# Performance work log

Measured on AMD Instinct MI355X. Metric: run time of the kernel, lower is better.

Reference implementation:

```python
import jax, jax.numpy as jnp
import numpy as np

LATENT, TARGET, EMB_SCALE = 2048, 64, 0.1
STEPS_IGNORE, STEPS_PREDICT = 2, 3


def conv(x, w, b, stride=(1, 1), padding=((0, 0), (0, 0))):
    y = jax.lax.conv_general_dilated(x, w, stride, padding,
                                     dimension_numbers=('NCHW', 'OIHW', 'NCHW'))
    return y + b[None, :, None, None]


def setup_inputs() -> dict:
    key = jax.random.key(0)
    ks = jax.random.split(key, 24)
    B = 64
    inp = {}
    inp['images'] = jax.random.normal(ks[0], (B, 3, 256, 256), jnp.float32)
    inp['rnd'] = jax.random.randint(ks[1], (B * 49,), 0, 16, jnp.int32)
    s = lambda *sh: 1.0 / np.sqrt(np.prod(sh[1:]))
    # stand-in encoder: conv3->256 k8 s8, relu, conv256->2048 1x1, relu, global mean pool
    inp['enc_w1'] = jax.random.normal(ks[2], (256, 3, 8, 8), jnp.float32) * s(256, 3, 8, 8)
    inp['enc_b1'] = jnp.zeros((256,), jnp.float32)
    inp['enc_w2'] = jax.random.normal(ks[3], (LATENT, 256, 1, 1), jnp.float32) * s(LATENT, 256)
    inp['enc_b2'] = jnp.zeros((LATENT,), jnp.float32)
    # PixelCNN: 5 residual blocks, each 4 convs
    inp['pc_w1'] = jax.random.normal(ks[4], (5, 256, LATENT, 1, 1), jnp.float32) * s(0, LATENT)
    inp['pc_b1'] = jnp.zeros((5, 256), jnp.float32)
    inp['pc_w2'] = jax.random.normal(ks[5], (5, 256, 256, 1, 3), jnp.float32) * s(0, 256 * 3)
    inp['pc_b2'] = jnp.zeros((5, 256), jnp.float32)
    inp['pc_w3'] = jax.random.normal(ks[6], (5, 256, 256, 2, 1), jnp.float32) * s(0, 256 * 2)
    inp['pc_b3'] = jnp.zeros((5, 256), jnp.float32)
    inp['pc_w4'] = jax.random.normal(ks[7], (5, LATENT, 256, 1, 1), jnp.float32) * s(0, 256)
    inp['pc_b4'] = jnp.zeros((5, LATENT), jnp.float32)
    inp['z2t_w'] = jax.random.normal(ks[8], (TARGET, LATENT, 1, 1), jnp.float32) * s(0, LATENT)
    inp['z2t_b'] = jnp.zeros((TARGET,), jnp.float32)
    inp['c2p_w'] = jax.random.normal(ks[9], (STEPS_PREDICT, TARGET, LATENT, 1, 1), jnp.float32) * s(0, LATENT)
    inp['c2p_b'] = jnp.zeros((STEPS_PREDICT, TARGET), jnp.float32)
    return inp


def _forward(images, enc_w1, enc_b1, enc_w2, enc_b2,
             pc_w1, pc_b1, pc_w2, pc_b2, pc_w3, pc_b3, pc_w4, pc_b4,
             z2t_w, z2t_b, c2p_w, c2p_b, rnd):
    B = images.shape[0]
    # ---- patch extraction: (B,3,256,256) -> (B*49,3,64,64), r-major then c ----
    patches = jnp.stack([images[:, :, r * 32:r * 32 + 64, c * 32:c * 32 + 64]
                         for r in range(7) for c in range(7)], axis=1)
    patches = patches.reshape(-1, 3, 64, 64)
    N = patches.shape[0]
    # ---- vectorized random border masking (replaces per-patch python loop) ----
    r = (rnd // 4).astype(jnp.int32)           # (N,)
    c = (rnd % 4).astype(jnp.int32)
    idx = jnp.arange(64, dtype=jnp.int32)
    row_ok = (idx[None, :] >= r[:, None]) & (idx[None, :] < r[:, None] + 60)  # (N,64)
    col_ok = (idx[None, :] >= c[:, None]) & (idx[None, :] < c[:, None] + 60)
    mask = row_ok[:, None, :, None] & col_ok[:, None, None, :]                # (N,1,64,64)
    patches = jnp.where(mask, patches, jnp.float32(-1.0))
    # ---- stand-in encoder (resnet_v1 replaced by small conv stack) ----
    h = jax.nn.relu(conv(patches, enc_w1, enc_b1, stride=(8, 8)))  # (N,256,8,8)
    h = jax.nn.relu(conv(h, enc_w2, enc_b2))                        # (N,2048,8,8)
    latents = h.mean(axis=(2, 3))                                   # (N,2048)
    latents = latents.reshape(B, 7, 7, LATENT).transpose(0, 3, 1, 2)  # (B,2048,7,7)
    # ---- PixelCNN context ----
    x = latents
    for k in range(5):
        y = jax.nn.relu(conv(x, pc_w1[k], pc_b1[k]))
        y = jax.nn.relu(conv(y, pc_w2[k], pc_b2[k], padding=((0, 0), (1, 1))))
        y = jax.nn.relu(conv(y, pc_w3[k], pc_b3[k], padding=((1, 0), (0, 0))))
        y = conv(y, pc_w4[k], pc_b4[k])
        x = jax.nn.relu(y + x)
    context = x
    # ---- contrastive loss ----
    targets = conv(latents, z2t_w, z2t_b).transpose(0, 2, 3, 1).reshape(-1, TARGET)  # (B*49,64)
    col_dim, row_dim = 7, 7
    loss = jnp.float32(0.0)
    for i in range(STEPS_IGNORE, STEPS_IGNORE + STEPS_PREDICT):
        col_dim_i = col_dim - i - 1
        total = B * col_dim_i * row_dim
        preds = conv(context, c2p_w[i - STEPS_IGNORE], c2p_b[i - STEPS_IGNORE])
        preds = preds[:, :, :-(i + 1), :] * EMB_SCALE
        preds = preds.transpose(0, 2, 3, 1).reshape(-1, TARGET)  # (total,64)
        logits = preds @ targets.T                                # (total, B*49)
        ar = jnp.arange(total)
        b_idx = ar // (col_dim_i * row_dim)
        col = ar % (col_dim_i * row_dim)
        labels = b_idx * (col_dim * row_dim) + (i + 1) * row_dim + col
        lsm = jax.nn.log_softmax(logits, axis=-1)
        loss = loss + (-lsm[ar, labels]).mean()
    return loss, latents.mean(axis=(2, 3))


def reference(images, rnd, enc_w1, enc_b1, enc_w2, enc_b2,
              pc_w1, pc_b1, pc_w2, pc_b2, pc_w3, pc_b3, pc_w4, pc_b4,
              z2t_w, z2t_b, c2p_w, c2p_b):
    return _forward(images, enc_w1, enc_b1, enc_w2, enc_b2,
                    pc_w1, pc_b1, pc_w2, pc_b2, pc_w3, pc_b3, pc_w4, pc_b4,
                    z2t_w, z2t_b, c2p_w, c2p_b, rnd)
```

## Files before the change

kernel.cpp:

```cpp
#include <hip/hip_runtime.h>
#include <hip/hip_bf16.h>
#include <cstdint>
#include <cstddef>

typedef __attribute__((ext_vector_type(8))) short short8;
typedef __attribute__((ext_vector_type(4))) short short4v;
typedef __attribute__((ext_vector_type(4))) float f32x4;

__device__ __forceinline__ float bf2f(unsigned short u) {
  union { unsigned int i; float f; } v; v.i = ((unsigned int)u) << 16; return v.f;
}
__device__ __forceinline__ unsigned short f2bf(float f) {
  union { float f; unsigned int i; } v; v.f = f;
  unsigned int x = v.i;
  return (unsigned short)((x + 0x7fffu + ((x >> 16) & 1u)) >> 16);
}
__device__ __forceinline__ f32x4 mfma16(short8 a, short8 b, f32x4 c) {
  return __builtin_amdgcn_mfma_f32_16x16x32_bf16(a, b, c, 0, 0, 0);
}
__device__ __forceinline__ void gload16(const void* src, void* dst) {
  __builtin_amdgcn_global_load_lds(
      (const __attribute__((address_space(1))) unsigned int*)src,
      (__attribute__((address_space(3))) unsigned int*)dst, 16, 0, 0);
}

__device__ __forceinline__ void cvt4(const float* __restrict__ src,
                                     unsigned short* __restrict__ dst, int i) {
  float4 v = reinterpret_cast<const float4*>(src)[i];
  short4v o;
  o[0] = (short)f2bf(v.x); o[1] = (short)f2bf(v.y);
  o[2] = (short)f2bf(v.z); o[3] = (short)f2bf(v.w);
  reinterpret_cast<short4v*>(dst)[i] = o;
}

__global__ __launch_bounds__(256) void k_prep(
    const float* __restrict__ enc_w1, const float* __restrict__ enc_w2,
    const float* __restrict__ pc_w1, const float* __restrict__ pc_w4,
    const float* __restrict__ z2t_w, const float* __restrict__ c2p_w,
    const float* __restrict__ pc_w2, const float* __restrict__ pc_w3,
    unsigned short* __restrict__ w1b, unsigned short* __restrict__ w2b,
    unsigned short* __restrict__ pcw1b, unsigned short* __restrict__ pcw4b,
    unsigned short* __restrict__ z2tb, unsigned short* __restrict__ c2pb,
    unsigned short* __restrict__ w2t, unsigned short* __restrict__ w3t)
{
  const int b = blockIdx.x, tid = threadIdx.x;
  if (b < 48)        cvt4(enc_w1, w1b,   b * 256 + tid);
  else if (b < 560)  cvt4(enc_w2, w2b,   (b - 48) * 256 + tid);
  else if (b < 3120) cvt4(pc_w1,  pcw1b, (b - 560) * 256 + tid);
  else if (b < 5680) cvt4(pc_w4,  pcw4b, (b - 3120) * 256 + tid);
  else if (b < 5808) cvt4(z2t_w,  z2tb,  (b - 5680) * 256 + tid);
  else if (b < 6192) cvt4(c2p_w,  c2pb,  (b - 5808) * 256 + tid);
  else if (b < 10032) {
    const int e = (b - 6192) * 256 + tid;
    const int k5 = e / 196608, r = e % 196608;
    const int co = r / 768, kk = r % 768, d = kk >> 8, ci = kk & 255;
    w2t[e] = f2bf(pc_w2[((size_t)(k5 * 256 + co) * 256 + ci) * 3 + d]);
  } else {
    const int e = (b - 10032) * 256 + tid;
    const int k5 = e / 131072, r = e % 131072;
    const int co = r >> 9, kk = r & 511, s = kk >> 8, ci = kk & 255;
    w3t[e] = f2bf(pc_w3[((size_t)(k5 * 256 + co) * 256 + ci) * 2 + s]);
  }
}

__global__ __launch_bounds__(256) void k_enc2(
    const unsigned short* __restrict__ H1, const unsigned short* __restrict__ w2b,
    const float* __restrict__ b2, unsigned short* __restrict__ xout, int gbase)
{
  __shared__ char lds[32768];
  char* At = lds;
  char* Bt = lds + 16384;
  const int tid = threadIdx.x;
  const int nwg = gridDim.x;
  int bid = blockIdx.x;
  int l = bid;
  if ((nwg & 7) == 0) { const int cpx = nwg >> 3; l = (bid & 7) * cpx + (bid >> 3); }
  const int m0 = (l & 15) * 128;
  const int by = l >> 4;
  const int w = tid >> 6, lane = tid & 63, lr = lane & 15, lg = lane >> 4;
  const int wm = w & 1, wn = w >> 1;
  const int srow = lane >> 3, sslot = lane & 7;
  f32x4 acc[4][4];
  for (int i = 0; i < 4; i++) for (int j = 0; j < 4; j++) acc[i][j] = (f32x4)0.f;
  for (int kb = 0; kb < 4; kb++) {
    __syncthreads();
#pragma unroll
    for (int c = 0; c < 4; c++) {
      const int rbase = w * 32 + c * 8;
      const int row = rbase + srow;
      gload16(w2b + (size_t)(m0 + row) * 256 + kb * 64 + ((sslot ^ (row & 7)) * 8),
              At + rbase * 128);
    }
#pragma unroll
    for (int c = 0; c < 4; c++) {
      const int rbase = w * 32 + c * 8;
      const int row = rbase + srow;
      gload16(H1 + (size_t)(by * 128 + row) * 256 + kb * 64 + ((sslot ^ (row & 7)) * 8),
              Bt + rbase * 128);
    }
    __syncthreads();
#pragma unroll
    for (int kk = 0; kk < 2; kk++) {
      const int gg = kk * 4 + lg;
      short8 bb[4];
#pragma unroll
      for (int nt = 0; nt < 4; nt++) {
        const int row = wn * 64 + nt * 16 + lr;
        bb[nt] = *reinterpret_cast<const short8*>(Bt + row * 128 + ((gg ^ (row & 7)) * 16));
      }
#pragma unroll
      for (int cot = 0; cot < 4; cot++) {
        const int row = wm * 64 + cot * 16 + lr;
        const short8 a = *reinterpret_cast<const short8*>(At + row * 128 + ((gg ^ (row & 7)) * 16));
#pragma unroll
        for (int nt = 0; nt < 4; nt++)
          acc[cot][nt] = mfma16(a, bb[nt], acc[cot][nt]);
      }
    }
  }
  const int n = gbase + by * 2 + wn;
#pragma unroll
  for (int cot = 0; cot < 4; cot++) {
    const int cob = m0 + wm * 64 + cot * 16 + lg * 4;
    float4 bi = *reinterpret_cast<const float4*>(b2 + cob);
    const float bv[4] = { bi.x, bi.y, bi.z, bi.w };
    float s[4] = { 0.f, 0.f, 0.f, 0.f };
#pragma unroll
    for (int nt = 0; nt < 4; nt++)
#pragma unroll
      for (int r = 0; r < 4; r++)
        s[r] += fmaxf(acc[cot][nt][r] + bv[r], 0.f);
#pragma unroll
    for (int r = 0; r < 4; r++)
#pragma unroll
      for (int mk = 1; mk < 16; mk <<= 1)
        s[r] += __shfl_xor(s[r], mk, 64);
    if (lr == 0) {
      short4v o;
#pragma unroll
      for (int r = 0; r < 4; r++) o[r] = (short)f2bf(s[r] * (1.f / 64.f));
      *reinterpret_cast<short4v*>(xout + (size_t)n * 2048 + cob) = o;
    }
  }
}

__global__ __launch_bounds__(256) void k_out2(const unsigned short* __restrict__ x,
                                              float* __restrict__ out) {
  const int ch = blockIdx.x * 256 + threadIdx.x;
  const int b = blockIdx.y;
  float s = 0.f;
  for (int p = 0; p < 49; p++) s += bf2f(x[(size_t)(b * 49 + p) * 2048 + ch]);
  out[1 + b * 2048 + ch] = s * (1.f / 49.f);
}

template<int M_BLK, int MODE, bool BIAS, bool RELU, bool RESID, bool SCALE, bool OBF16>
__global__ __launch_bounds__(256) void k_gemm(
    const unsigned short* __restrict__ in, const unsigned short* __restrict__ W,
    const float* __restrict__ bias, float* __restrict__ outf,
    unsigned short* __restrict__ outb, const unsigned short* __restrict__ res,
    int M, int K, int bstride, int aux, float scale,
    int wzs, int bzs, int ozs,
    const float* __restrict__ img, const int* __restrict__ rndp)
{
  constexpr int MF = M_BLK / 64;
  constexpr int AG = M_BLK * 8;
  constexpr int CHA = M_BLK / 32;
  __shared__ char ldsb[(M_BLK + 64) * 128];
  char* At = ldsb;
  char* Bt = ldsb + M_BLK * 128;
  const int tid = threadIdx.x;
  const int z = blockIdx.z;
  W += (size_t)z * wzs;
  if (BIAS) bias += (size_t)z * bzs;
  const int m0 = blockIdx.x * M_BLK;
  const int n0 = blockIdx.y * 64;
  const int w = tid >> 6, lane = tid & 63, lr = lane & 15, lg = lane >> 4;
  const int srow = lane >> 3, sslot = lane & 7;
  int pb = 0, pR = 0, pC = 0, roff = 0, coff = 0;
  if constexpr (MODE == 4) {
    const int pn = aux + blockIdx.y;
    pb = pn / 49; const int prc = pn % 49; pR = prc / 7; pC = prc % 7;
    const int rv = rndp[pn];
    roff = rv >> 2; coff = rv & 3;
  }
  f32x4 acc[MF][4];
  for (int mf = 0; mf < MF; mf++) for (int nt = 0; nt < 4; nt++) acc[mf][nt] = (f32x4)0.f;
  const int KB = K >> 6;
  for (int kb = 0; kb < KB; kb++) {
    __syncthreads();
#pragma unroll
    for (int c = 0; c < CHA; c++) {
      const int rbase = w * (M_BLK / 4) + c * 8;
      const int row = rbase + srow;
      gload16(W + (size_t)(m0 + row) * K + kb * 64 + ((sslot ^ (row & 7)) * 8),
              At + rbase * 128);
    }
    if constexpr (MODE == 0 || MODE == 3) {
#pragma unroll
      for (int c = 0; c < 2; c++) {
        const int rbase = w * 16 + c * 8;
        const int row = rbase + srow;
        int n = n0 + row;
        if constexpr (MODE == 3) n = (n / aux) * 49 + (n % aux);
        gload16(in + (size_t)n * bstride + kb * 64 + ((sslot ^ (row & 7)) * 8),
                Bt + rbase * 128);
      }
    } else {
      for (int g = AG + tid; g < AG + 512; g += 256) {
        const int h = g - AG, row = h >> 3, slot = h & 7;
        const int n = n0 + row;
        const int k = kb * 64 + slot * 8;
        short8 v = (short8)(short)0;
        if constexpr (MODE == 1) {
          const int d = k >> 8, ci = k & 255;
          const int wp = n % 7 + d - 1;
          if ((unsigned)wp <= 6u)
            v = *reinterpret_cast<const short8*>(in + (size_t)(n + d - 1) * 256 + ci);
        } else if constexpr (MODE == 2) {
          const int s2 = k >> 8, ci = k & 255;
          const int hh = (n % 49) / 7;
          if (hh + s2 >= 1)
            v = *reinterpret_cast<const short8*>(in + (size_t)(n + (s2 - 1) * 7) * 256 + ci);
        } else {
          const int p = row;
          const int gr = kb * 8 + slot;
          const int ci = gr >> 3, ky = gr & 7;
          const int oy = p >> 3, ox = p & 7;
          const int y = oy * 8 + ky;
          const float* src = img + (((size_t)(pb * 3 + ci) * 256 + (size_t)(pR * 32 + y)) * 256
                                    + pC * 32 + ox * 8);
          float4 v0 = *reinterpret_cast<const float4*>(src);
          float4 v1 = *reinterpret_cast<const float4*>(src + 4);
          const bool rok = (y >= roff) && (y < roff + 60);
          float vals[8] = { v0.x, v0.y, v0.z, v0.w, v1.x, v1.y, v1.z, v1.w };
          const int x0 = ox * 8;
#pragma unroll
          for (int q = 0; q < 8; q++) {
            const int xx = x0 + q;
            const bool ok = rok && (xx >= coff) && (xx < coff + 60);
            v[q] = (short)f2bf(ok ? vals[q] : -1.0f);
          }
        }
        *reinterpret_cast<short8*>(Bt + row * 128 + ((slot ^ (row & 7)) * 16)) = v;
      }
    }
    __syncthreads();
#pragma unroll
    for (int kk = 0; kk < 2; kk++) {
      short8 a[MF], bb[4];
      const int gg = kk * 4 + lg;
#pragma unroll
      for (int mf = 0; mf < MF; mf++) {
        const int row = w * (M_BLK / 4) + mf * 16 + lr;
        a[mf] = *reinterpret_cast<const short8*>(At + row * 128 + ((gg ^ (row & 7)) * 16));
      }
#pragma unroll
      for (int nt = 0; nt < 4; nt++) {
        const int row = nt * 16 + lr;
        bb[nt] = *reinterpret_cast<const short8*>(Bt + row * 128 + ((gg ^ (row & 7)) * 16));
      }
#pragma unroll
      for (int mf = 0; mf < MF; mf++)
#pragma unroll
        for (int nt = 0; nt < 4; nt++)
          acc[mf][nt] = mfma16(a[mf], bb[nt], acc[mf][nt]);
    }
  }
#pragma unroll
  for (int mf = 0; mf < MF; mf++) {
    const int mb = m0 + w * (M_BLK / 4) + mf * 16 + lg * 4;
    float bv[4] = {0.f, 0.f, 0.f, 0.f};
    if constexpr (BIAS) {
      float4 t4 = *reinterpret_cast<const float4*>(bias + mb);
      bv[0] = t4.x; bv[1] = t4.y; bv[2] = t4.z; bv[3] = t4.w;
    }
#pragma unroll
    for (int nt = 0; nt < 4; nt++) {
      const size_t nn = (size_t)(n0 + nt * 16 + lr);
      const size_t off = nn * (size_t)M + mb + (size_t)z * ozs;
      float v[4];
#pragma unroll
      for (int r = 0; r < 4; r++) {
        v[r] = acc[mf][nt][r] + bv[r];
        if (SCALE) v[r] *= scale;
      }
      if (RESID) {
        short4v rv = *reinterpret_cast<const short4v*>(res + off);
#pragma unroll
        for (int r = 0; r < 4; r++) v[r] += bf2f((unsigned short)rv[r]);
      }
#pragma unroll
      for (int r = 0; r < 4; r++) if (RELU) v[r] = fmaxf(v[r], 0.f);
      if (OBF16) {
        short4v o;
#pragma unroll
        for (int r = 0; r < 4; r++) o[r] = (short)f2bf(v[r]);
        *reinterpret_cast<short4v*>(outb + off) = o;
      } else {
        float4 o; o.x = v[0]; o.y = v[1]; o.z = v[2]; o.w = v[3];
        *reinterpret_cast<float4*>(outf + off) = o;
      }
    }
  }
}

__global__ __launch_bounds__(256) void k_lse(const float* __restrict__ logits,
                                             float* __restrict__ lossr,
                                             int cd7, int base, int lab7)
{
  __shared__ float redM[256], redS[256];
  const int r = blockIdx.x, tid = threadIdx.x;
  const float4* row = reinterpret_cast<const float4*>(logits + (size_t)r * 3136);
  float m = -1e30f, s = 0.f;
  for (int i = tid; i < 784; i += 256) {
    float4 v4 = row[i];
    float vv[4] = { v4.x, v4.y, v4.z, v4.w };
#pragma unroll
    for (int q = 0; q < 4; q++) {
      const float nm = fmaxf(m, vv[q]);
      s = s * __expf(m - nm) + __expf(vv[q] - nm);
      m = nm;
    }
  }
  redM[tid] = m; redS[tid] = s;
  for (int off = 128; off > 0; off >>= 1) {
    __syncthreads();
    if (tid < off) {
      const float m2 = redM[tid + off], s2 = redS[tid + off];
      const float nm = fmaxf(redM[tid], m2);
      redS[tid] = redS[tid] * __expf(redM[tid] - nm) + s2 * __expf(m2 - nm);
      redM[tid] = nm;
    }
  }
  __syncthreads();
  if (tid == 0) {
    const int b = r / cd7, hw = r % cd7;
    const int lab = b * 49 + hw + lab7;
    lossr[base + r] = (redM[0] + __logf(redS[0])) - logits[(size_t)r * 3136 + lab];
  }
}

__global__ __launch_bounds__(256) void k_loss_final(const float* __restrict__ lossr,
                                                    float* __restrict__ out) {
  __shared__ float red[256];
  const int tid = threadIdx.x;
  float s = 0.f;
  for (int i = tid; i < 4032; i += 256) {
    const float wgt = (i < 1792) ? (1.f / 1792.f) : ((i < 3136) ? (1.f / 1344.f) : (1.f / 896.f));
    s += lossr[i] * wgt;
  }
  red[tid] = s;
  for (int off = 128; off > 0; off >>= 1) {
    __syncthreads();
    if (tid < off) red[tid] += red[tid + off];
  }
  if (tid == 0) out[0] = red[0];
}

extern "C" void kernel_launch(void* const* d_in, const int* in_sizes, int n_in,
                              void* d_out, int out_size, void* d_ws, size_t ws_size,
                              hipStream_t stream)
{
  (void)in_sizes; (void)n_in; (void)out_size;
  const float* images = (const float*)d_in[0];
  const int*   rnd    = (const int*)d_in[1];
  const float* enc_w1 = (const float*)d_in[2];
  const float* enc_b1 = (const float*)d_in[3];
  const float* enc_w2 = (const float*)d_in[4];
  const float* enc_b2 = (const float*)d_in[5];
  const float* pc_w1  = (const float*)d_in[6];
  const float* pc_b1  = (const float*)d_in[7];
  const float* pc_w2  = (const float*)d_in[8];
  const float* pc_b2  = (const float*)d_in[9];
  const float* pc_w3  = (const float*)d_in[10];
  const float* pc_b3  = (const float*)d_in[11];
  const float* pc_w4  = (const float*)d_in[12];
  const float* pc_b4  = (const float*)d_in[13];
  const float* z2t_w  = (const float*)d_in[14];
  const float* z2t_b  = (const float*)d_in[15];
  const float* c2p_w  = (const float*)d_in[16];
  const float* c2p_b  = (const float*)d_in[17];
  float* out = (float*)d_out;
  char* ws = (char*)d_ws;

  unsigned short* w1b    = (unsigned short*)(ws + 0);
  unsigned short* w2b    = (unsigned short*)(ws + 98304);
  unsigned short* z2tb   = (unsigned short*)(ws + 1146880);
  unsigned short* c2pb   = (unsigned short*)(ws + 1409024);
  unsigned short* w2t    = (unsigned short*)(ws + 2195456);
  unsigned short* w3t    = (unsigned short*)(ws + 4161536);
  unsigned short* targ   = (unsigned short*)(ws + 5472256);
  unsigned short* predsb = (unsigned short*)(ws + 5873664);
  float*          lossr  = (float*)(ws + 7077888);
  unsigned short* y1b    = (unsigned short*)(ws + 7094016);
  unsigned short* y2b    = (unsigned short*)(ws + 8699648);
  unsigned short* pcw1b  = (unsigned short*)(ws + 10305280);
  unsigned short* pcw4b  = (unsigned short*)(ws + 15548160);
  unsigned short* xbuf   = (unsigned short*)(ws + 20791040);
  float*          logits = (float*)(ws + 10305280);

  k_prep<<<12592, 256, 0, stream>>>(enc_w1, enc_w2, pc_w1, pc_w4, z2t_w, c2p_w,
                                    pc_w2, pc_w3,
                                    w1b, w2b, pcw1b, pcw4b, z2tb, c2pb, w2t, w3t);

  const size_t h1_off = 33636352;
  const size_t per_patch = 64 * 256 * 2;
  unsigned short* H1;
  int CH;
  if (ws_size > h1_off + 2 * per_patch) {
    size_t avail = (ws_size - h1_off) / per_patch;
    CH = (int)(avail > 3136 ? 3136 : avail) & ~1;
    H1 = (unsigned short*)(ws + h1_off);
  } else {
    H1 = y1b;
    CH = 98;
  }
  for (int base = 0; base < 3136; base += CH) {
    const int c = (3136 - base) < CH ? (3136 - base) : CH;
    k_gemm<256, 4, true, true, false, false, true><<<dim3(1, c), 256, 0, stream>>>(
        nullptr, w1b, enc_b1, nullptr, H1, nullptr, 256, 192, 0, base, 1.f,
        0, 0, 0, images, rnd);
    k_enc2<<<16 * (c / 2), 256, 0, stream>>>(H1, w2b, enc_b2, xbuf, base);
  }

  k_out2<<<dim3(8, 64), 256, 0, stream>>>(xbuf, out);
  k_gemm<64, 0, true, false, false, false, true><<<dim3(1, 49), 256, 0, stream>>>(
      xbuf, z2tb, z2t_b, nullptr, targ, nullptr, 64, 2048, 2048, 0, 1.f, 0, 0, 0,
      nullptr, nullptr);

  for (int k = 0; k < 5; k++) {
    k_gemm<64, 0, true, true, false, false, true><<<dim3(4, 49), 256, 0, stream>>>(
        xbuf, pcw1b + (size_t)k * 524288, pc_b1 + k * 256, nullptr, y1b, nullptr,
        256, 2048, 2048, 0, 1.f, 0, 0, 0, nullptr, nullptr);
    k_gemm<64, 1, true, true, false, false, true><<<dim3(4, 49), 256, 0, stream>>>(
        y1b, w2t + (size_t)k * 196608, pc_b2 + k * 256, nullptr, y2b, nullptr,
        256, 768, 256, 0, 1.f, 0, 0, 0, nullptr, nullptr);
    k_gemm<64, 2, true, true, false, false, true><<<dim3(4, 49), 256, 0, stream>>>(
        y2b, w3t + (size_t)k * 131072, pc_b3 + k * 256, nullptr, y1b, nullptr,
        256, 512, 256, 0, 1.f, 0, 0, 0, nullptr, nullptr);
    k_gemm<128, 0, true, true, true, false, true><<<dim3(16, 49), 256, 0, stream>>>(
        y1b, pcw4b + (size_t)k * 524288, pc_b4 + k * 2048, nullptr, xbuf, xbuf,
        2048, 256, 256, 0, 1.f, 0, 0, 0, nullptr, nullptr);
  }

  k_gemm<64, 0, true, false, false, true, true><<<dim3(1, 49, 3), 256, 0, stream>>>(
      xbuf, c2pb, c2p_b, nullptr, predsb, nullptr, 64, 2048, 2048, 0, 0.1f,
      131072, 64, 200704, nullptr, nullptr);

  const int cd7a[3] = {28, 21, 14};
  const int basea[3] = {0, 1792, 3136};
  for (int ip = 0; ip < 3; ip++) {
    const int rows = cd7a[ip] * 64;
    k_gemm<64, 3, false, false, false, false, false><<<dim3(49, rows / 64), 256, 0, stream>>>(
        predsb + (size_t)ip * 200704, targ, nullptr, logits, nullptr, nullptr,
        3136, 64, 64, cd7a[ip], 1.f, 0, 0, 0, nullptr, nullptr);
    k_lse<<<rows, 256, 0, stream>>>(logits, lossr, cd7a[ip], basea[ip], 7 * (ip + 3));
  }
  k_loss_final<<<1, 256, 0, stream>>>(lossr, out);
}
```

Baseline: 723.9 us.

## Double-buffer LDS tiles in encoder and GEMM kernels to overlap loads with MFMA

Adds ping-pong LDS buffers to k_enc2 and to the k_gemm modes that load B tiles with direct global-to-LDS copies (modes 0 and 3). The next K-tile is issued into the spare buffer before the MFMA loop on the current tile, and one barrier per iteration replaces two. The aim is to hide global load latency behind the matrix math. In exchange, LDS use per block doubles, which can cut how many workgroups fit on a CU. The modes that gather B tiles in software keep the single-buffer path.

```diff
diff --git a/kernel.cpp b/kernel.cpp
--- a/kernel.cpp
+++ b/kernel.cpp
@@ -67,9 +67,7 @@
     const unsigned short* __restrict__ H1, const unsigned short* __restrict__ w2b,
     const float* __restrict__ b2, unsigned short* __restrict__ xout, int gbase)
 {
-  __shared__ char lds[32768];
-  char* At = lds;
-  char* Bt = lds + 16384;
+  __shared__ char lds[2][32768];
   const int tid = threadIdx.x;
   const int nwg = gridDim.x;
   int bid = blockIdx.x;
@@ -82,8 +80,10 @@
   const int srow = lane >> 3, sslot = lane & 7;
   f32x4 acc[4][4];
   for (int i = 0; i < 4; i++) for (int j = 0; j < 4; j++) acc[i][j] = (f32x4)0.f;
-  for (int kb = 0; kb < 4; kb++) {
-    __syncthreads();
+
+  auto STAGE = [&](int buf, int kb) {
+    char* At = lds[buf];
+    char* Bt = lds[buf] + 16384;
 #pragma unroll
     for (int c = 0; c < 4; c++) {
       const int rbase = w * 32 + c * 8;
@@ -98,7 +98,15 @@
       gload16(H1 + (size_t)(by * 128 + row) * 256 + kb * 64 + ((sslot ^ (row & 7)) * 8),
               Bt + rbase * 128);
     }
-    __syncthreads();
+  };
+
+  STAGE(0, 0);
+  __syncthreads();
+  int cur = 0;
+  for (int kb = 0; kb < 4; kb++) {
+    if (kb < 3) STAGE(cur ^ 1, kb + 1);
+    char* At = lds[cur];
+    char* Bt = lds[cur] + 16384;
 #pragma unroll
     for (int kk = 0; kk < 2; kk++) {
       const int gg = kk * 4 + lg;
@@ -117,6 +125,8 @@
           acc[cot][nt] = mfma16(a, bb[nt], acc[cot][nt]);
       }
     }
+    __syncthreads();
+    cur ^= 1;
   }
   const int n = gbase + by * 2 + wn;
 #pragma unroll
@@ -165,9 +175,9 @@
   constexpr int MF = M_BLK / 64;
   constexpr int AG = M_BLK * 8;
   constexpr int CHA = M_BLK / 32;
-  __shared__ char ldsb[(M_BLK + 64) * 128];
-  char* At = ldsb;
-  char* Bt = ldsb + M_BLK * 128;
+  constexpr bool DBUF = (MODE == 0 || MODE == 3);
+  constexpr int BUF = (M_BLK + 64) * 128;
+  __shared__ char ldsb[(DBUF ? 2 : 1) * BUF];
   const int tid = threadIdx.x;
   const int z = blockIdx.z;
   W += (size_t)z * wzs;
@@ -186,8 +196,8 @@
   f32x4 acc[MF][4];
   for (int mf = 0; mf < MF; mf++) for (int nt = 0; nt < 4; nt++) acc[mf][nt] = (f32x4)0.f;
   const int KB = K >> 6;
-  for (int kb = 0; kb < KB; kb++) {
-    __syncthreads();
+
+  auto stageA = [&](char* At, int kb) {
 #pragma unroll
     for (int c = 0; c < CHA; c++) {
       const int rbase = w * (M_BLK / 4) + c * 8;
@@ -195,7 +205,32 @@
       gload16(W + (size_t)(m0 + row) * K + kb * 64 + ((sslot ^ (row & 7)) * 8),
               At + rbase * 128);
     }
-    if constexpr (MODE == 0 || MODE == 3) {
+  };
+  auto compute = [&](const char* At, const char* Bt) {
+#pragma unroll
+    for (int kk = 0; kk < 2; kk++) {
+      short8 a[MF], bb[4];
+      const int gg = kk * 4 + lg;
+#pragma unroll
+      for (int mf = 0; mf < MF; mf++) {
+        const int row = w * (M_BLK / 4) + mf * 16 + lr;
+        a[mf] = *reinterpret_cast<const short8*>(At + row * 128 + ((gg ^ (row & 7)) * 16));
+      }
+#pragma unroll
+      for (int nt = 0; nt < 4; nt++) {
+        const int row = nt * 16 + lr;
+        bb[nt] = *reinterpret_cast<const short8*>(Bt + row * 128 + ((gg ^ (row & 7)) * 16));
+      }
+#pragma unroll
+      for (int mf = 0; mf < MF; mf++)
+#pragma unroll
+        for (int nt = 0; nt < 4; nt++)
+          acc[mf][nt] = mfma16(a[mf], bb[nt], acc[mf][nt]);
+    }
+  };
+
+  if constexpr (DBUF) {
+    auto stageB = [&](char* Bt, int kb) {
 #pragma unroll
       for (int c = 0; c < 2; c++) {
         const int rbase = w * 16 + c * 8;
@@ -205,7 +240,27 @@
         gload16(in + (size_t)n * bstride + kb * 64 + ((sslot ^ (row & 7)) * 8),
                 Bt + rbase * 128);
       }
-    } else {
+    };
+    stageA(ldsb, 0);
+    stageB(ldsb + M_BLK * 128, 0);
+    __syncthreads();
+    int cur = 0;
+    for (int kb = 0; kb < KB; kb++) {
+      if (kb + 1 < KB) {
+        char* nb = ldsb + (cur ^ 1) * BUF;
+        stageA(nb, kb + 1);
+        stageB(nb + M_BLK * 128, kb + 1);
+      }
+      char* cb = ldsb + cur * BUF;
+      compute(cb, cb + M_BLK * 128);
+      __syncthreads();
+      cur ^= 1;
+    }
+  } else {
+    for (int kb = 0; kb < KB; kb++) {
+      __syncthreads();
+      stageA(ldsb, kb);
+      char* Bt = ldsb + M_BLK * 128;
       for (int g = AG + tid; g < AG + 512; g += 256) {
         const int h = g - AG, row = h >> 3, slot = h & 7;
         const int n = n0 + row;
@@ -243,29 +298,11 @@
         }
         *reinterpret_cast<short8*>(Bt + row * 128 + ((slot ^ (row & 7)) * 16)) = v;
       }
-    }
-    __syncthreads();
-#pragma unroll
-    for (int kk = 0; kk < 2; kk++) {
-      short8 a[MF], bb[4];
-      const int gg = kk * 4 + lg;
-#pragma unroll
-      for (int mf = 0; mf < MF; mf++) {
-        const int row = w * (M_BLK / 4) + mf * 16 + lr;
-        a[mf] = *reinterpret_cast<const short8*>(At + row * 128 + ((gg ^ (row & 7)) * 16));
-      }
-#pragma unroll
-      for (int nt = 0; nt < 4; nt++) {
-        const int row = nt * 16 + lr;
-        bb[nt] = *reinterpret_cast<const short8*>(Bt + row * 128 + ((gg ^ (row & 7)) * 16));
-      }
-#pragma unroll
-      for (int mf = 0; mf < MF; mf++)
-#pragma unroll
-        for (int nt = 0; nt < 4; nt++)
-          acc[mf][nt] = mfma16(a[mf], bb[nt], acc[mf][nt]);
-    }
-  }
+      __syncthreads();
+      compute(ldsb, ldsb + M_BLK * 128);
+    }
+  }
+
 #pragma unroll
   for (int mf = 0; mf < MF; mf++) {
     const int mb = m0 + w * (M_BLK / 4) + mf * 16 + lg * 4;
```

New measurement: 749.7 us. 1.04x slower.
